# Optimization experiments

Hardware: AMD Instinct MI355X
Metric: run time of the kernel (lower is better)

## Reference

```python
import jax, jax.numpy as jnp
import numpy as np

NUM_HEADS = 16
ROPE_THETA = 10000.0
RMS_EPS = 1e-6


def _rope(t):
    # t: [B, L, H, D]; standard interleaved rotary embedding over sequence positions
    B, L, H, D = t.shape
    half = D // 2
    inv_freq = 1.0 / (ROPE_THETA ** (jnp.arange(half, dtype=jnp.float32) / half))
    ang = jnp.arange(L, dtype=jnp.float32)[:, None] * inv_freq[None, :]  # [L, half]
    cos = jnp.cos(ang)[None, :, None, :]  # [1, L, 1, half]
    sin = jnp.sin(ang)[None, :, None, :]
    t1 = t[..., 0::2]
    t2 = t[..., 1::2]
    r1 = t1 * cos - t2 * sin
    r2 = t1 * sin + t2 * cos
    out = jnp.stack([r1, r2], axis=-1).reshape(B, L, H, D)
    return out


def _qk_rms_norm(t, gamma):
    # t: [B, L, H, D]; gamma: [H, D] learned scale per head-channel
    rms = jnp.sqrt(jnp.mean(jnp.square(t), axis=-1, keepdims=True) + RMS_EPS)
    return (t / rms) * gamma[None, None, :, :]


def setup_inputs() -> dict:
    key = jax.random.key(0)
    ks = jax.random.split(key, 5)
    B, L, C = 2, 2048, 1024
    x = jax.random.normal(ks[0], (B, L, C), dtype=jnp.float32)
    w_qkv = jax.random.normal(ks[1], (3 * C, C), dtype=jnp.float32) * 0.02
    b_qkv = jax.random.normal(ks[2], (3 * C,), dtype=jnp.float32) * 0.02
    w_out = jax.random.normal(ks[3], (C, C), dtype=jnp.float32) * 0.02
    b_out = jax.random.normal(ks[4], (C,), dtype=jnp.float32) * 0.02
    q_gamma = jnp.ones((NUM_HEADS, C // NUM_HEADS), dtype=jnp.float32)
    k_gamma = jnp.ones((NUM_HEADS, C // NUM_HEADS), dtype=jnp.float32)
    return {"x": x, "w_qkv": w_qkv, "b_qkv": b_qkv, "w_out": w_out,
            "b_out": b_out, "q_gamma": q_gamma, "k_gamma": k_gamma}


def reference(x, w_qkv, b_qkv, w_out, b_out, q_gamma, k_gamma):
    B, L, C = x.shape
    H = NUM_HEADS
    D = C // H
    # fused QKV projection -> [B, L, 3, H, D]
    qkv = (x @ w_qkv.T + b_qkv).reshape(B, L, 3, H, D)
    q, k, v = qkv[:, :, 0], qkv[:, :, 1], qkv[:, :, 2]  # each [B, L, H, D]
    # inline RoPE on q, k
    q = _rope(q)
    k = _rope(k)
    # QK RMSNorm with learned per-head scale
    q = _qk_rms_norm(q, q_gamma)
    k = _qk_rms_norm(k, k_gamma)
    # full (non-causal) scaled dot-product attention
    scale = 1.0 / jnp.sqrt(jnp.float32(D))
    scores = jnp.einsum('blhd,bmhd->bhlm', q, k) * scale  # [B, H, L, L]
    attn = jax.nn.softmax(scores, axis=-1)
    o = jnp.einsum('bhlm,bmhd->blhd', attn, v).reshape(B, L, C)
    return o @ w_out.T + b_out
```

## Files before the change

### kernel.cpp

```cpp
#include <hip/hip_runtime.h>
#include <stdint.h>

typedef __attribute__((ext_vector_type(8))) short short8;
typedef __attribute__((ext_vector_type(4))) float f32x4;
typedef __attribute__((ext_vector_type(16))) float f32x16;

#define LOG2E 1.44269504088896f

__device__ __forceinline__ float bf2f(uint16_t u) {
    union { uint32_t i; float f; } v; v.i = ((uint32_t)u) << 16; return v.f;
}
__device__ __forceinline__ uint16_t f2bf(float f) {
    union { float f; uint32_t i; } v; v.f = f;
    return (uint16_t)((v.i + 0x7fffu + ((v.i >> 16) & 1u)) >> 16);
}

__global__ void cast_kernel(const float4* __restrict__ in, uint64_t* __restrict__ out, int n4) {
    int stride = gridDim.x * blockDim.x;
    for (int i = blockIdx.x * blockDim.x + threadIdx.x; i < n4; i += stride) {
        float4 v = in[i];
        uint64_t o = (uint64_t)f2bf(v.x) | ((uint64_t)f2bf(v.y) << 16)
                   | ((uint64_t)f2bf(v.z) << 32) | ((uint64_t)f2bf(v.w) << 48);
        out[i] = o;
    }
}

__global__ void rope_table_kernel(float2* __restrict__ tab) {
    int idx = blockIdx.x * 256 + threadIdx.x;
    int l = idx >> 5, i = idx & 31;
    float fr = powf(10000.0f, -(float)i * (1.0f / 32.0f));
    float ang = (float)l * fr;
    float s, c;
    sincosf(ang, &s, &c);
    tab[idx] = make_float2(c, s);
}

template<bool OUTBF>
__global__ __launch_bounds__(256, 2) void gemm_bt(
    const uint16_t* __restrict__ A, const uint16_t* __restrict__ Bw,
    const float* __restrict__ bias, void* __restrict__ outp,
    int M, int N, int K)
{
    __shared__ uint16_t Asm[128 * 64];
    __shared__ uint16_t Bsm[128 * 64];
    int tid = threadIdx.x;
    int wave = tid >> 6, lane = tid & 63;
    int bm = blockIdx.y * 128, bn = blockIdx.x * 128;
    int wm = (wave >> 1) * 64, wn = (wave & 1) * 64;

    f32x4 acc[4][4] = {};

    int srow = lane >> 3;
    int sc16 = lane & 7;

    for (int k0 = 0; k0 < K; k0 += 64) {
#pragma unroll
        for (int c = 0; c < 4; ++c) {
            int chunk = wave * 4 + c;
            int row = chunk * 8 + srow;
            int col = ((sc16 ^ (row & 7)) << 3);
            __builtin_amdgcn_global_load_lds(
                (const __attribute__((address_space(1))) void*)(A + (size_t)(bm + row) * K + k0 + col),
                (__attribute__((address_space(3))) void*)(Asm + chunk * 512),
                16, 0, 0);
            __builtin_amdgcn_global_load_lds(
                (const __attribute__((address_space(1))) void*)(Bw + (size_t)(bn + row) * K + k0 + col),
                (__attribute__((address_space(3))) void*)(Bsm + chunk * 512),
                16, 0, 0);
        }
        __syncthreads();
#pragma unroll
        for (int kk = 0; kk < 2; ++kk) {
            short8 af[4], bfr[4];
#pragma unroll
            for (int m = 0; m < 4; ++m) {
                int row = wm + m * 16 + (lane & 15);
                int kc = kk * 4 + (lane >> 4);
                af[m] = *(const short8*)(Asm + row * 64 + ((kc ^ (row & 7)) << 3));
            }
#pragma unroll
            for (int n = 0; n < 4; ++n) {
                int row = wn + n * 16 + (lane & 15);
                int kc = kk * 4 + (lane >> 4);
                bfr[n] = *(const short8*)(Bsm + row * 64 + ((kc ^ (row & 7)) << 3));
            }
#pragma unroll
            for (int m = 0; m < 4; ++m)
#pragma unroll
                for (int n = 0; n < 4; ++n)
                    acc[m][n] = __builtin_amdgcn_mfma_f32_16x16x32_bf16(af[m], bfr[n], acc[m][n], 0, 0, 0);
        }
        __syncthreads();
    }
#pragma unroll
    for (int m = 0; m < 4; ++m) {
#pragma unroll
        for (int n = 0; n < 4; ++n) {
            int col = bn + wn + n * 16 + (lane & 15);
            float bv = bias[col];
#pragma unroll
            for (int r = 0; r < 4; ++r) {
                int row = bm + wm + m * 16 + (lane >> 4) * 4 + r;
                float val = acc[m][n][r] + bv;
                if (OUTBF) ((uint16_t*)outp)[(size_t)row * N + col] = f2bf(val);
                else       ((float*)outp)[(size_t)row * N + col] = val;
            }
        }
    }
}

__global__ void rope_rms_kernel(const uint16_t* __restrict__ qkv, const float2* __restrict__ tab,
                                const float* __restrict__ qg, const float* __restrict__ kg,
                                uint16_t* __restrict__ Q, uint16_t* __restrict__ Kk, uint16_t* __restrict__ V)
{
    int bl = blockIdx.x;
    int h = blockIdx.y * 4 + (threadIdx.x >> 6);
    int d = threadIdx.x & 63;
    int l = bl & 2047;
    const uint16_t* base = qkv + (size_t)bl * 3072 + h * 64;
    size_t outoff = ((((size_t)(bl >> 11)) * 16 + h) * 2048 + l) * 64 + d;

    V[outoff] = base[2048 + d];

    float2 cs = tab[l * 32 + (d >> 1)];
    float sg = (d & 1) ? cs.y : -cs.y;
    {
        float t = bf2f(base[d]);
        float p = bf2f(base[d ^ 1]);
        float r = t * cs.x + p * sg;
        float ss = r * r;
#pragma unroll
        for (int m = 32; m >= 1; m >>= 1) ss += __shfl_xor(ss, m);
        float scale = rsqrtf(ss * (1.0f / 64.0f) + 1e-6f) * qg[h * 64 + d] * (0.125f * LOG2E);
        Q[outoff] = f2bf(r * scale);
    }
    {
        float t = bf2f(base[1024 + d]);
        float p = bf2f(base[1024 + (d ^ 1)]);
        float r = t * cs.x + p * sg;
        float ss = r * r;
#pragma unroll
        for (int m = 32; m >= 1; m >>= 1) ss += __shfl_xor(ss, m);
        float scale = rsqrtf(ss * (1.0f / 64.0f) + 1e-6f) * kg[h * 64 + d];
        Kk[outoff] = f2bf(r * scale);
    }
}

__global__ __launch_bounds__(512, 4) void flash_kernel(
    const uint16_t* __restrict__ Q, const uint16_t* __restrict__ K, const uint16_t* __restrict__ V,
    uint16_t* __restrict__ O)
{
    __shared__ __align__(16) uint16_t lds[32768];
    int tid = threadIdx.x, wave = tid >> 6, lane = tid & 63;
    int qw = wave & 3, half = wave >> 2;
    uint16_t* Ksm = lds + half * 16384;
    uint16_t* Vsm = Ksm + 8192;

    int lq = lane & 31;
    int hi = lane >> 5;
    int bh = blockIdx.y;
    int q0 = blockIdx.x * 128 + qw * 32;
    int kvbase = half * 1024;
    const uint16_t* Qb = Q + (size_t)bh * 2048 * 64;
    const uint16_t* Kb = K + (size_t)bh * 2048 * 64;
    const uint16_t* Vb = V + (size_t)bh * 2048 * 64;

    short8 qf[4];
#pragma unroll
    for (int kb = 0; kb < 4; ++kb)
        qf[kb] = *(const short8*)(Qb + (size_t)(q0 + lq) * 64 + kb * 16 + hi * 8);

    f32x16 oacc0 = {}, oacc1 = {};
    float lsum = 0.0f;

    int tid_h = tid & 255;
    int kvp = tid_h & 31, dg = tid_h >> 5;
    int r8 = lane >> 3, sl = lane & 7;
    int srccol = (sl ^ r8) << 3;

#pragma unroll
    for (int c = 0; c < 2; ++c) {
        int ch = qw * 2 + c;
        __builtin_amdgcn_global_load_lds(
            (const __attribute__((address_space(1))) void*)(Kb + (size_t)(kvbase + ch * 8 + r8) * 64 + srccol),
            (__attribute__((address_space(3))) void*)(Ksm + ch * 512), 16, 0, 0);
    }
    short8 va  = *(const short8*)(Vb + (size_t)(kvbase + kvp * 2) * 64 + dg * 8);
    short8 vb2 = *(const short8*)(Vb + (size_t)(kvbase + kvp * 2 + 1) * 64 + dg * 8);

    int buf = 0;
    for (int t = 0; t < 16; ++t) {
        {
            char* Vbase = (char*)(Vsm + buf * 4096);
#pragma unroll
            for (int j = 0; j < 8; ++j) {
                uint32_t wd = (uint32_t)(uint16_t)va[j] | ((uint32_t)(uint16_t)vb2[j] << 16);
                *(uint32_t*)(Vbase + (dg * 8 + j) * 128 + (((kvp >> 2) ^ j) << 4) + ((kvp & 3) << 2)) = wd;
            }
        }
        __syncthreads();

        if (t < 15) {
            int kv0n = kvbase + (t + 1) * 64;
#pragma unroll
            for (int c = 0; c < 2; ++c) {
                int ch = qw * 2 + c;
                __builtin_amdgcn_global_load_lds(
                    (const __attribute__((address_space(1))) void*)(Kb + (size_t)(kv0n + ch * 8 + r8) * 64 + srccol),
                    (__attribute__((address_space(3))) void*)(Ksm + (buf ^ 1) * 4096 + ch * 512), 16, 0, 0);
            }
            va  = *(const short8*)(Vb + (size_t)(kv0n + kvp * 2) * 64 + dg * 8);
            vb2 = *(const short8*)(Vb + (size_t)(kv0n + kvp * 2 + 1) * 64 + dg * 8);
        }

        const uint16_t* Kbase = Ksm + buf * 4096;
        f32x16 st0 = {}, st1 = {};
        __builtin_amdgcn_s_setprio(1);
#pragma unroll
        for (int kb = 0; kb < 4; ++kb) {
            int sw = ((hi + 2 * kb) ^ (lq & 7)) << 3;
            short8 kf0 = *(const short8*)(Kbase + lq * 64 + sw);
            short8 kf1 = *(const short8*)(Kbase + (32 + lq) * 64 + sw);
            st0 = __builtin_amdgcn_mfma_f32_32x32x16_bf16(kf0, qf[kb], st0, 0, 0, 0);
            st1 = __builtin_amdgcn_mfma_f32_32x32x16_bf16(kf1, qf[kb], st1, 0, 0, 0);
        }
        __builtin_amdgcn_s_setprio(0);

        float rs0 = 0.0f, rs1 = 0.0f;
        uint32_t w0[4][2], w1[4][2];
#pragma unroll
        for (int qd = 0; qd < 4; ++qd) {
#pragma unroll
            for (int k2 = 0; k2 < 2; ++k2) {
                float a0 = exp2f(st0[qd * 4 + k2 * 2]);
                float a1 = exp2f(st0[qd * 4 + k2 * 2 + 1]);
                rs0 += a0 + a1;
                asm("v_cvt_pk_bf16_f32 %0, %1, %2" : "=v"(w0[qd][k2]) : "v"(a0), "v"(a1));
                float b0 = exp2f(st1[qd * 4 + k2 * 2]);
                float b1 = exp2f(st1[qd * 4 + k2 * 2 + 1]);
                rs1 += b0 + b1;
                asm("v_cvt_pk_bf16_f32 %0, %1, %2" : "=v"(w1[qd][k2]) : "v"(b0), "v"(b1));
            }
        }
        lsum += rs0 + rs1;

        __builtin_amdgcn_s_setprio(1);
#pragma unroll
        for (int c = 0; c < 4; ++c) {
            int s = c & 1;
            uint32_t A0, B0, A1, B1;
            if (c < 2) { A0 = w0[s * 2][0]; B0 = w0[s * 2 + 1][0]; A1 = w0[s * 2][1]; B1 = w0[s * 2 + 1][1]; }
            else       { A0 = w1[s * 2][0]; B0 = w1[s * 2 + 1][0]; A1 = w1[s * 2][1]; B1 = w1[s * 2 + 1][1]; }
            asm volatile("v_permlane32_swap_b32 %0, %1" : "+v"(A0), "+v"(B0));
            asm volatile("v_permlane32_swap_b32 %0, %1" : "+v"(A1), "+v"(B1));
            union { uint32_t u[4]; short8 s8; } pu;
            pu.u[0] = A0; pu.u[1] = A1; pu.u[2] = B0; pu.u[3] = B1;
            int sw = ((2 * c + hi) ^ (lq & 7)) << 3;
            const uint16_t* Vbase = Vsm + buf * 4096;
            short8 vf0 = *(const short8*)(Vbase + lq * 64 + sw);
            short8 vf1 = *(const short8*)(Vbase + (32 + lq) * 64 + sw);
            oacc0 = __builtin_amdgcn_mfma_f32_32x32x16_bf16(vf0, pu.s8, oacc0, 0, 0, 0);
            oacc1 = __builtin_amdgcn_mfma_f32_32x32x16_bf16(vf1, pu.s8, oacc1, 0, 0, 0);
        }
        __builtin_amdgcn_s_setprio(0);
        buf ^= 1;
    }

    lsum += __shfl_xor(lsum, 32);
    __syncthreads();
    float* cb = (float*)lds;
    if (half == 1) {
        int b0 = qw * 33 * 64;
#pragma unroll
        for (int i = 0; i < 16; ++i) cb[b0 + i * 64 + lane] = oacc0[i];
#pragma unroll
        for (int i = 0; i < 16; ++i) cb[b0 + (16 + i) * 64 + lane] = oacc1[i];
        cb[b0 + 32 * 64 + lane] = lsum;
    }
    __syncthreads();
    if (half == 1) return;
    {
        int b0 = qw * 33 * 64;
#pragma unroll
        for (int i = 0; i < 16; ++i) oacc0[i] += cb[b0 + i * 64 + lane];
#pragma unroll
        for (int i = 0; i < 16; ++i) oacc1[i] += cb[b0 + (16 + i) * 64 + lane];
        lsum += cb[b0 + 32 * 64 + lane];
    }

    float inv = 1.0f / lsum;
    char* Osm = (char*)(lds + 18432) + qw * 4608;
#pragma unroll
    for (int qd = 0; qd < 4; ++qd) {
#pragma unroll
        for (int k2 = 0; k2 < 2; ++k2) {
            int dbase = 8 * qd + 4 * hi + 2 * k2;
            float p0 = oacc0[qd * 4 + k2 * 2] * inv, p1 = oacc0[qd * 4 + k2 * 2 + 1] * inv;
            uint32_t wd;
            asm("v_cvt_pk_bf16_f32 %0, %1, %2" : "=v"(wd) : "v"(p0), "v"(p1));
            *(uint32_t*)(Osm + lq * 144 + dbase * 2) = wd;
            float p2 = oacc1[qd * 4 + k2 * 2] * inv, p3 = oacc1[qd * 4 + k2 * 2 + 1] * inv;
            asm("v_cvt_pk_bf16_f32 %0, %1, %2" : "=v"(wd) : "v"(p2), "v"(p3));
            *(uint32_t*)(Osm + lq * 144 + (32 + dbase) * 2) = wd;
        }
    }
    asm volatile("s_waitcnt lgkmcnt(0)" ::: "memory");
    int q2 = lane >> 1, hf = lane & 1;
    size_t orow = (size_t)((bh >> 4) * 2048 + blockIdx.x * 128 + qw * 32 + q2) * 1024
                + (size_t)(bh & 15) * 64 + hf * 32;
#pragma unroll
    for (int ch = 0; ch < 4; ++ch) {
        short8 o = *(const short8*)(Osm + q2 * 144 + hf * 64 + ch * 16);
        *(short8*)(O + orow + ch * 8) = o;
    }
}

extern "C" void kernel_launch(void* const* d_in, const int* in_sizes, int n_in,
                              void* d_out, int out_size, void* d_ws, size_t ws_size,
                              hipStream_t stream)
{
    const float* x      = (const float*)d_in[0];
    const float* w_qkv  = (const float*)d_in[1];
    const float* b_qkv  = (const float*)d_in[2];
    const float* w_out  = (const float*)d_in[3];
    const float* b_out  = (const float*)d_in[4];
    const float* qg     = (const float*)d_in[5];
    const float* kg     = (const float*)d_in[6];
    float* out = (float*)d_out;

    char* w = (char*)d_ws;
    uint16_t* x_bf    = (uint16_t*)w;  w += (size_t)4096 * 1024 * 2;
    uint16_t* wqkv_bf = (uint16_t*)w;  w += (size_t)3072 * 1024 * 2;
    uint16_t* wout_bf = (uint16_t*)w;  w += (size_t)1024 * 1024 * 2;
    float2*   tab     = (float2*)w;    w += (size_t)2048 * 32 * 8;
    uint16_t* qkv_bf  = (uint16_t*)w;  w += (size_t)4096 * 3072 * 2;
    uint16_t* Qb      = (uint16_t*)w;  w += (size_t)4096 * 1024 * 2;
    uint16_t* Kb      = (uint16_t*)w;  w += (size_t)4096 * 1024 * 2;
    uint16_t* Vb      = (uint16_t*)w;  w += (size_t)4096 * 1024 * 2;
    uint16_t* attn_bf = (uint16_t*)w;  w += (size_t)4096 * 1024 * 2;

    cast_kernel<<<2048, 256, 0, stream>>>((const float4*)x,     (uint64_t*)x_bf,    4096 * 1024 / 4);
    cast_kernel<<<2048, 256, 0, stream>>>((const float4*)w_qkv, (uint64_t*)wqkv_bf, 3072 * 1024 / 4);
    cast_kernel<<<1024, 256, 0, stream>>>((const float4*)w_out, (uint64_t*)wout_bf, 1024 * 1024 / 4);
    rope_table_kernel<<<256, 256, 0, stream>>>(tab);

    gemm_bt<true><<<dim3(24, 32), 256, 0, stream>>>(x_bf, wqkv_bf, b_qkv, qkv_bf, 4096, 3072, 1024);
    rope_rms_kernel<<<dim3(4096, 4), 256, 0, stream>>>(qkv_bf, tab, qg, kg, Qb, Kb, Vb);
    flash_kernel<<<dim3(16, 32), 512, 0, stream>>>(Qb, Kb, Vb, attn_bf);
    gemm_bt<false><<<dim3(8, 32), 256, 0, stream>>>(attn_bf, wout_bf, b_out, out, 4096, 1024, 1024);
}
```

Measured before the change: 232.7 us.

## Split flash attention KV halves into separate blocks with a combine kernel

Each 512-thread flash block used to process both KV halves in two wave groups and reduce them through LDS. Now each KV half runs as its own 256-thread block (grid z=2), which halves LDS per block and doubles the block count to improve occupancy and scheduling. Each block writes unnormalized bf16 partial outputs and row sums into reused workspace, and a new combine kernel adds the halves and normalizes. In exchange this adds an extra kernel launch, extra global traffic for the partials, and an extra bf16 rounding of the unnormalized partials.

New measurement: 236.4 us. No clear change (+1.6%).

```diff
diff --git a/kernel.cpp b/kernel.cpp
--- a/kernel.cpp
+++ b/kernel.cpp
@@ -146,21 +146,21 @@
     }
 }
 
-__global__ __launch_bounds__(512, 4) void flash_kernel(
+__global__ __launch_bounds__(256, 4) void flash_kernel(
     const uint16_t* __restrict__ Q, const uint16_t* __restrict__ K, const uint16_t* __restrict__ V,
-    uint16_t* __restrict__ O)
-{
-    __shared__ __align__(16) uint16_t lds[32768];
+    uint16_t* __restrict__ Opart, float* __restrict__ lsums)
+{
+    __shared__ __align__(16) uint16_t lds[16384];
+    uint16_t* Ksm = lds;
+    uint16_t* Vsm = lds + 8192;
+
     int tid = threadIdx.x, wave = tid >> 6, lane = tid & 63;
-    int qw = wave & 3, half = wave >> 2;
-    uint16_t* Ksm = lds + half * 16384;
-    uint16_t* Vsm = Ksm + 8192;
-
     int lq = lane & 31;
     int hi = lane >> 5;
     int bh = blockIdx.y;
-    int q0 = blockIdx.x * 128 + qw * 32;
-    int kvbase = half * 1024;
+    int half = blockIdx.z;
+    int q0 = blockIdx.x * 128 + wave * 32;
+    int kvbase = half << 10;
     const uint16_t* Qb = Q + (size_t)bh * 2048 * 64;
     const uint16_t* Kb = K + (size_t)bh * 2048 * 64;
     const uint16_t* Vb = V + (size_t)bh * 2048 * 64;
@@ -173,14 +173,13 @@
     f32x16 oacc0 = {}, oacc1 = {};
     float lsum = 0.0f;
 
-    int tid_h = tid & 255;
-    int kvp = tid_h & 31, dg = tid_h >> 5;
+    int kvp = tid & 31, dg = tid >> 5;
     int r8 = lane >> 3, sl = lane & 7;
     int srccol = (sl ^ r8) << 3;
 
 #pragma unroll
     for (int c = 0; c < 2; ++c) {
-        int ch = qw * 2 + c;
+        int ch = wave * 2 + c;
         __builtin_amdgcn_global_load_lds(
             (const __attribute__((address_space(1))) void*)(Kb + (size_t)(kvbase + ch * 8 + r8) * 64 + srccol),
             (__attribute__((address_space(3))) void*)(Ksm + ch * 512), 16, 0, 0);
@@ -204,7 +203,7 @@
             int kv0n = kvbase + (t + 1) * 64;
 #pragma unroll
             for (int c = 0; c < 2; ++c) {
-                int ch = qw * 2 + c;
+                int ch = wave * 2 + c;
                 __builtin_amdgcn_global_load_lds(
                     (const __attribute__((address_space(1))) void*)(Kb + (size_t)(kv0n + ch * 8 + r8) * 64 + srccol),
                     (__attribute__((address_space(3))) void*)(Ksm + (buf ^ 1) * 4096 + ch * 512), 16, 0, 0);
@@ -267,52 +266,52 @@
     }
 
     lsum += __shfl_xor(lsum, 32);
+    if (lane < 32)
+        lsums[(size_t)half * 65536 + (size_t)bh * 2048 + q0 + lq] = lsum;
     __syncthreads();
-    float* cb = (float*)lds;
-    if (half == 1) {
-        int b0 = qw * 33 * 64;
-#pragma unroll
-        for (int i = 0; i < 16; ++i) cb[b0 + i * 64 + lane] = oacc0[i];
-#pragma unroll
-        for (int i = 0; i < 16; ++i) cb[b0 + (16 + i) * 64 + lane] = oacc1[i];
-        cb[b0 + 32 * 64 + lane] = lsum;
-    }
-    __syncthreads();
-    if (half == 1) return;
-    {
-        int b0 = qw * 33 * 64;
-#pragma unroll
-        for (int i = 0; i < 16; ++i) oacc0[i] += cb[b0 + i * 64 + lane];
-#pragma unroll
-        for (int i = 0; i < 16; ++i) oacc1[i] += cb[b0 + (16 + i) * 64 + lane];
-        lsum += cb[b0 + 32 * 64 + lane];
-    }
-
-    float inv = 1.0f / lsum;
-    char* Osm = (char*)(lds + 18432) + qw * 4608;
+    char* Osm = (char*)(lds + wave * 2304);
 #pragma unroll
     for (int qd = 0; qd < 4; ++qd) {
 #pragma unroll
         for (int k2 = 0; k2 < 2; ++k2) {
             int dbase = 8 * qd + 4 * hi + 2 * k2;
-            float p0 = oacc0[qd * 4 + k2 * 2] * inv, p1 = oacc0[qd * 4 + k2 * 2 + 1] * inv;
             uint32_t wd;
-            asm("v_cvt_pk_bf16_f32 %0, %1, %2" : "=v"(wd) : "v"(p0), "v"(p1));
+            asm("v_cvt_pk_bf16_f32 %0, %1, %2" : "=v"(wd)
+                : "v"(oacc0[qd * 4 + k2 * 2]), "v"(oacc0[qd * 4 + k2 * 2 + 1]));
             *(uint32_t*)(Osm + lq * 144 + dbase * 2) = wd;
-            float p2 = oacc1[qd * 4 + k2 * 2] * inv, p3 = oacc1[qd * 4 + k2 * 2 + 1] * inv;
-            asm("v_cvt_pk_bf16_f32 %0, %1, %2" : "=v"(wd) : "v"(p2), "v"(p3));
+            asm("v_cvt_pk_bf16_f32 %0, %1, %2" : "=v"(wd)
+                : "v"(oacc1[qd * 4 + k2 * 2]), "v"(oacc1[qd * 4 + k2 * 2 + 1]));
             *(uint32_t*)(Osm + lq * 144 + (32 + dbase) * 2) = wd;
         }
     }
     asm volatile("s_waitcnt lgkmcnt(0)" ::: "memory");
     int q2 = lane >> 1, hf = lane & 1;
-    size_t orow = (size_t)((bh >> 4) * 2048 + blockIdx.x * 128 + qw * 32 + q2) * 1024
+    size_t orow = (size_t)half * 4194304
+                + (size_t)((bh >> 4) * 2048 + blockIdx.x * 128 + wave * 32 + q2) * 1024
                 + (size_t)(bh & 15) * 64 + hf * 32;
 #pragma unroll
     for (int ch = 0; ch < 4; ++ch) {
         short8 o = *(const short8*)(Osm + q2 * 144 + hf * 64 + ch * 16);
-        *(short8*)(O + orow + ch * 8) = o;
-    }
+        *(short8*)(Opart + orow + ch * 8) = o;
+    }
+}
+
+__global__ void combine_kernel(const uint16_t* __restrict__ part, const float* __restrict__ lsums,
+                               uint16_t* __restrict__ out)
+{
+    int i = blockIdx.x * 256 + threadIdx.x;
+    int bl = i >> 7, c8 = i & 127;
+    int b = bl >> 11, l = bl & 2047, h = c8 >> 3;
+    short8 p0 = *(const short8*)(part + (size_t)bl * 1024 + c8 * 8);
+    short8 p1 = *(const short8*)(part + 4194304 + (size_t)bl * 1024 + c8 * 8);
+    float l0 = lsums[(b * 16 + h) * 2048 + l];
+    float l1 = lsums[65536 + (b * 16 + h) * 2048 + l];
+    float inv = 1.0f / (l0 + l1);
+    short8 o;
+#pragma unroll
+    for (int j = 0; j < 8; ++j)
+        o[j] = (short)f2bf((bf2f((uint16_t)p0[j]) + bf2f((uint16_t)p1[j])) * inv);
+    *(short8*)(out + (size_t)bl * 1024 + c8 * 8) = o;
 }
 
 extern "C" void kernel_launch(void* const* d_in, const int* in_sizes, int n_in,
@@ -339,6 +338,9 @@
     uint16_t* Vb      = (uint16_t*)w;  w += (size_t)4096 * 1024 * 2;
     uint16_t* attn_bf = (uint16_t*)w;  w += (size_t)4096 * 1024 * 2;
 
+    uint16_t* part  = qkv_bf;
+    float*    lsums = (float*)tab;
+
     cast_kernel<<<2048, 256, 0, stream>>>((const float4*)x,     (uint64_t*)x_bf,    4096 * 1024 / 4);
     cast_kernel<<<2048, 256, 0, stream>>>((const float4*)w_qkv, (uint64_t*)wqkv_bf, 3072 * 1024 / 4);
     cast_kernel<<<1024, 256, 0, stream>>>((const float4*)w_out, (uint64_t*)wout_bf, 1024 * 1024 / 4);
@@ -346,6 +348,7 @@
 
     gemm_bt<true><<<dim3(24, 32), 256, 0, stream>>>(x_bf, wqkv_bf, b_qkv, qkv_bf, 4096, 3072, 1024);
     rope_rms_kernel<<<dim3(4096, 4), 256, 0, stream>>>(qkv_bf, tab, qg, kg, Qb, Kb, Vb);
-    flash_kernel<<<dim3(16, 32), 512, 0, stream>>>(Qb, Kb, Vb, attn_bf);
+    flash_kernel<<<dim3(16, 32, 2), 256, 0, stream>>>(Qb, Kb, Vb, part, lsums);
+    combine_kernel<<<2048, 256, 0, stream>>>(part, lsums, attn_bf);
     gemm_bt<false><<<dim3(8, 32), 256, 0, stream>>>(attn_bf, wout_bf, b_out, out, 4096, 1024, 1024);
 }
```
